# Optimization experiments

Hardware: AMD Instinct MI355X
Metric: run time of the kernel (lower is better)

The kernel has to match this reference:

```python
import jax, jax.numpy as jnp
import numpy as np

B, N, F = 4, 1024, 512        # batch, tokens, features
H, D = 8, 64                  # heads, attention_dim (= value dim here)
E = 16                        # edge feature dim
LN_EPS = 1e-5


def setup_inputs() -> dict:
    key = jax.random.key(0)
    ks = jax.random.split(key, 9)
    receiver_input = jax.random.normal(ks[0], (B, N, F), dtype=jnp.float32)
    edge_features = jax.random.normal(ks[1], (B, N, N, E), dtype=jnp.float32)
    mask = (jax.random.uniform(ks[2], (B, N, N)) > 0.5).astype(jnp.float32)
    s = 1.0 / np.sqrt(F)
    Wq = jax.random.normal(ks[3], (F, H * D), dtype=jnp.float32) * s
    Wk = jax.random.normal(ks[4], (F, H * D), dtype=jnp.float32) * s
    Wv = jax.random.normal(ks[5], (F, H * D), dtype=jnp.float32) * s
    We = jax.random.normal(ks[6], (E, H), dtype=jnp.float32) * (1.0 / np.sqrt(E))
    Wo = jax.random.normal(ks[7], (H * D, H * D), dtype=jnp.float32) * (1.0 / np.sqrt(H * D))
    ln_scale = jnp.ones((F,), dtype=jnp.float32)
    ln_offset = jnp.zeros((F,), dtype=jnp.float32)
    return {
        "receiver_input": receiver_input, "edge_features": edge_features,
        "mask": mask, "ln_scale": ln_scale, "ln_offset": ln_offset,
        "Wq": Wq, "Wk": Wk, "Wv": Wv, "We": We, "Wo": Wo,
    }


def _layer_norm(x, scale, offset):
    mu = jnp.mean(x, axis=-1, keepdims=True)
    var = jnp.var(x, axis=-1, keepdims=True)
    return (x - mu) * jax.lax.rsqrt(var + LN_EPS) * scale + offset


def reference(receiver_input, edge_features, mask, ln_scale, ln_offset, Wq, Wk, Wv, We, Wo):
    r = _layer_norm(receiver_input, ln_scale, ln_offset)   # sender = receiver (self-attn)
    q = (r @ Wq).reshape(B, N, H, D)
    k = (r @ Wk).reshape(B, N, H, D)
    v = (r @ Wv).reshape(B, N, H, D)
    # logits [b, i, j, h]; edge bias added BEFORE softmax (over senders j = axis -2)
    logits = jnp.einsum("bihf,bjhf->bijh", q, k) + edge_features @ We
    w = jax.nn.softmax(logits, axis=-2)
    w = w * mask[..., None]                                 # post-softmax mask multiply
    out = jnp.einsum("bijh,bjhv->bihv", w, v)
    out = out.reshape(B, N, H * D) * (1.0 / jnp.sqrt(jnp.float32(D)))
    out = out @ Wo
    out = out + receiver_input                              # residual (shapes match: F == H*D)
    return out
```

## Files before the change

kernel.cpp:

```cpp
#include <hip/hip_runtime.h>

#define BB 4
#define NN 1024
#define FF 512
#define HH 8
#define DD 64
#define EE 16

typedef unsigned short u16;
typedef _Float16 f16;
typedef __attribute__((ext_vector_type(8))) _Float16 f16x8;
typedef __attribute__((ext_vector_type(4))) _Float16 f16x4;
typedef __attribute__((ext_vector_type(4))) float     f32x4;

#define MFMAH(a,b,c) __builtin_amdgcn_mfma_f32_16x16x32_f16((a),(b),(c),0,0,0)

static __device__ __forceinline__ void gld16(const void* g, void* l){
  __builtin_amdgcn_global_load_lds((const __attribute__((address_space(1))) unsigned int*)g,
                                   (__attribute__((address_space(3))) unsigned int*)l, 16, 0, 0);
}

__global__ __launch_bounds__(256) void k_wsplit(
    const float* __restrict__ Wq, const float* __restrict__ Wk,
    const float* __restrict__ Wv, const float* __restrict__ Wo,
    f16* __restrict__ WT, f16* __restrict__ WoT){
  __shared__ float tile[32][33];
  int bid = blockIdx.x, t = threadIdx.x;
  int isA = bid < 768;
  int tb  = isA ? bid : bid - 768;
  int nct = isA ? 48 : 16;
  int ct = tb % nct, ft = tb / nct;
  int c0 = ct * 32, f0 = ft * 32;
  #pragma unroll
  for (int r4 = 0; r4 < 4; r4++){
    int fl = (t >> 5) * 4 + r4, cl = t & 31;
    int f = f0 + fl, c = c0 + cl;
    float v;
    if (isA){
      const float* W = (c < 512) ? Wq : ((c < 1024) ? Wk : Wv);
      v = W[f * 512 + (c & 511)];
    } else {
      v = Wo[f * 512 + c];
    }
    tile[fl][cl] = v;
  }
  __syncthreads();
  #pragma unroll
  for (int r4 = 0; r4 < 4; r4++){
    int cl = (t >> 5) * 4 + r4, fl = t & 31;
    float v = tile[fl][cl];
    int c = c0 + cl, f = f0 + fl;
    if (isA) WT[c * 512 + f]  = (f16)v;
    else     WoT[c * 512 + f] = (f16)v;
  }
}

__global__ __launch_bounds__(256) void k_ln(
    const float* __restrict__ x, const float* __restrict__ gamma,
    const float* __restrict__ beta, f16* __restrict__ rf){
  int row  = blockIdx.x * 4 + (threadIdx.x >> 6);
  int lane = threadIdx.x & 63;
  const float* px = x + (size_t)row * 512 + lane * 8;
  float4 a = *(const float4*)px;
  float4 b = *(const float4*)(px + 4);
  float v[8] = {a.x,a.y,a.z,a.w,b.x,b.y,b.z,b.w};
  float s = 0.f, q = 0.f;
  #pragma unroll
  for (int j = 0; j < 8; j++){ s += v[j]; q += v[j]*v[j]; }
  #pragma unroll
  for (int m = 1; m < 64; m <<= 1){ s += __shfl_xor(s, m, 64); q += __shfl_xor(q, m, 64); }
  float mean = s * (1.f/512.f);
  float var  = q * (1.f/512.f) - mean * mean;
  float rstd = rsqrtf(var + 1e-5f);
  float4 ga = *(const float4*)(gamma + lane*8);
  float4 gb = *(const float4*)(gamma + lane*8 + 4);
  float4 b0 = *(const float4*)(beta  + lane*8);
  float4 b1 = *(const float4*)(beta  + lane*8 + 4);
  float gs[8] = {ga.x,ga.y,ga.z,ga.w,gb.x,gb.y,gb.z,gb.w};
  float bs[8] = {b0.x,b0.y,b0.z,b0.w,b1.x,b1.y,b1.z,b1.w};
  f16x8 hv;
  #pragma unroll
  for (int j = 0; j < 8; j++){
    float r = (v[j] - mean) * rstd * gs[j] + bs[j];
    hv[j] = (f16)r;
  }
  *(f16x8*)(rf + (size_t)row * 512 + lane * 8) = hv;
}

__global__ __launch_bounds__(256) void k_qkv(
    const f16* __restrict__ rf, const f16* __restrict__ WT,
    f16* __restrict__ qf, f16* __restrict__ kf, f16* __restrict__ vT){
  __shared__ f16 As[128*32], Bs[128*32];
  int bid = blockIdx.x;
  int mt = bid & 31, nt = bid >> 5;
  int m0 = mt << 7,  n0 = nt << 7;
  int t = threadIdx.x, lane = t & 63, w = t >> 6;
  int wm = (w >> 1) << 6, wn = (w & 1) << 6;
  int fr = lane & 15, g = lane >> 4;
  f32x4 acc[4][4];
  #pragma unroll
  for (int i = 0; i < 4; i++)
    #pragma unroll
    for (int j = 0; j < 4; j++) acc[i][j] = (f32x4){0.f,0.f,0.f,0.f};

  for (int k0 = 0; k0 < 512; k0 += 32){
    #pragma unroll
    for (int q = 0; q < 2; q++){
      int c = ((q << 2) + w) * 64 + lane;
      int row = c >> 2, part = c & 3;
      int ldso = ((q << 2) + w) * 512;
      gld16(rf + (size_t)(m0+row)*512 + k0 + part*8, &As[ldso]);
      gld16(WT + (size_t)(n0+row)*512 + k0 + part*8, &Bs[ldso]);
    }
    __syncthreads();
    f16x8 a[4], b[4];
    #pragma unroll
    for (int mi = 0; mi < 4; mi++) a[mi] = *(const f16x8*)&As[(wm + mi*16 + fr)*32 + g*8];
    #pragma unroll
    for (int ni = 0; ni < 4; ni++) b[ni] = *(const f16x8*)&Bs[(wn + ni*16 + fr)*32 + g*8];
    #pragma unroll
    for (int mi = 0; mi < 4; mi++)
      #pragma unroll
      for (int ni = 0; ni < 4; ni++)
        acc[mi][ni] = MFMAH(a[mi], b[ni], acc[mi][ni]);
    __syncthreads();
  }
  #pragma unroll
  for (int mi = 0; mi < 4; mi++)
    #pragma unroll
    for (int ni = 0; ni < 4; ni++)
      #pragma unroll
      for (int r = 0; r < 4; r++){
        int gm = m0 + wm + mi*16 + g*4 + r;
        int gc = n0 + wn + ni*16 + fr;
        float vv = acc[mi][ni][r];
        int b = gm >> 10, i = gm & 1023;
        int mat = gc >> 9, h = (gc >> 6) & 7, d = gc & 63;
        size_t idx = ((size_t)((b << 3) + h) * 1024 + i) * 64 + d;
        if      (mat == 0) qf[idx] = (f16)vv;
        else if (mat == 1) kf[idx] = (f16)vv;
        else vT[((size_t)((b << 3) + h) * 64 + d) * 1024 + i] = (f16)vv;
      }
}

__global__ __launch_bounds__(256) void k_bias(
    const float* __restrict__ edge, const float* __restrict__ We,
    f16* __restrict__ biasP){
  __shared__ char outb[4][1280];
  int t = threadIdx.x, lane = t & 63, w = t >> 6;
  int c = lane & 3, vq = lane >> 2;
  float wr[4][8];
  #pragma unroll
  for (int r = 0; r < 4; r++){
    float4 wa = *(const float4*)(We + (c*4 + r)*8);
    float4 wb = *(const float4*)(We + (c*4 + r)*8 + 4);
    wr[r][0]=wa.x; wr[r][1]=wa.y; wr[r][2]=wa.z; wr[r][3]=wa.w;
    wr[r][4]=wb.x; wr[r][5]=wb.y; wr[r][6]=wb.z; wr[r][7]=wb.w;
  }
  int bid = blockIdx.x;
  int i = bid & 1023, b = bid >> 10;
  const float* erow = edge + (size_t)bid * 16384;
  int h = lane >> 3, vb = lane & 7;
  f16* obase = biasP + (size_t)(b*8 + h) * 1048576 + (size_t)i * 1024;

  auto process = [&](const float4* e, int bt){
    #pragma unroll
    for (int n = 0; n < 4; n++){
      float p[8];
      #pragma unroll
      for (int hh = 0; hh < 8; hh++)
        p[hh] = e[n].x*wr[0][hh] + e[n].y*wr[1][hh] + e[n].z*wr[2][hh] + e[n].w*wr[3][hh];
      #pragma unroll
      for (int hh = 0; hh < 8; hh++){
        p[hh] += __shfl_xor(p[hh], 1, 64);
        p[hh] += __shfl_xor(p[hh], 2, 64);
      }
      unsigned lo = (unsigned)__builtin_bit_cast(u16, (f16)p[2*c]);
      unsigned hi = (unsigned)__builtin_bit_cast(u16, (f16)p[2*c + 1]);
      *(unsigned*)(&outb[w][(n*16 + vq)*20 + c*4]) = lo | (hi << 16);
    }
    asm volatile("s_waitcnt lgkmcnt(0)" ::: "memory");
    __builtin_amdgcn_sched_barrier(0);
    f16x8 ov;
    #pragma unroll
    for (int q = 0; q < 8; q++)
      ov[q] = __builtin_bit_cast(f16, *(const u16*)(&outb[w][(vb*8 + q)*20 + h*2]));
    *(f16x8*)(obase + (w*16 + bt*4)*16 + vb*8) = ov;
    asm volatile("s_waitcnt lgkmcnt(0)" ::: "memory");
    __builtin_amdgcn_sched_barrier(0);
  };

  float4 eA[4], eB[4];
  #pragma unroll
  for (int n = 0; n < 4; n++)
    eA[n] = *(const float4*)(erow + (size_t)(w*16 + n)*256 + lane*4);
  #pragma unroll
  for (int n = 0; n < 4; n++)
    eB[n] = *(const float4*)(erow + (size_t)(w*16 + 4 + n)*256 + lane*4);
  process(eA, 0);
  #pragma unroll
  for (int n = 0; n < 4; n++)
    eA[n] = *(const float4*)(erow + (size_t)(w*16 + 8 + n)*256 + lane*4);
  process(eB, 1);
  #pragma unroll
  for (int n = 0; n < 4; n++)
    eB[n] = *(const float4*)(erow + (size_t)(w*16 + 12 + n)*256 + lane*4);
  process(eA, 2);
  process(eB, 3);
}

__global__ __launch_bounds__(256) void k_attn(
    const f16* __restrict__ biasP, const float* __restrict__ mask,
    const f16* __restrict__ qf, const f16* __restrict__ kf,
    const f16* __restrict__ vT, f16* __restrict__ part_o,
    float2* __restrict__ part_md){
  __shared__ f16 pm_s[4][16*40];
  int t = threadIdx.x, lane = t & 63, w = t >> 6;
  int wid = blockIdx.x * 4 + w;
  int s = wid & 1, it = (wid >> 1) & 63, h = (wid >> 7) & 7, b = wid >> 10;
  int fr = lane & 15, g = lane >> 4;
  int bh = b*8 + h;

  size_t qb = ((size_t)bh * 1024 + it*16 + fr) * 64 + g*8;
  f16x8 qf0 = *(const f16x8*)(qf + qb);
  f16x8 qf1 = *(const f16x8*)(qf + qb + 32);

  const f16*   bbase = biasP + ((size_t)bh * 1024 + it*16) * 1024;
  const float* mbase = mask + (size_t)(b*1024 + it*16) * 1024;
  const f16*   kbase = kf + (size_t)bh * 65536;
  const f16*   vbase = vT + (size_t)bh * 65536;

  f32x4 oacc[4];
  #pragma unroll
  for (int vf = 0; vf < 4; vf++) oacc[vf] = (f32x4){0.f,0.f,0.f,0.f};
  float mrun[4], den[4];
  #pragma unroll
  for (int r = 0; r < 4; r++){ mrun[r] = -3e38f; den[r] = 0.f; }

  #pragma unroll 1
  for (int jt = s*16; jt < s*16 + 16; jt++){
    int j0 = jt << 5;
    const f16* kp = kbase + (size_t)(j0 + fr) * 64 + g*8;
    f16x8 kf00 = *(const f16x8*)(kp);
    f16x8 kf01 = *(const f16x8*)(kp + 32);
    f16x8 kf10 = *(const f16x8*)(kp + 16*64);
    f16x8 kf11 = *(const f16x8*)(kp + 16*64 + 32);
    f16x8 vfr[4];
    #pragma unroll
    for (int vf = 0; vf < 4; vf++)
      vfr[vf] = *(const f16x8*)(vbase + (size_t)(vf*16 + fr) * 1024 + j0 + g*8);
    float bs0[4], bs1[4], ms0[4], ms1[4];
    #pragma unroll
    for (int r = 0; r < 4; r++){
      int row = g*4 + r;
      bs0[r] = (float)bbase[(size_t)row*1024 + j0 + fr];
      bs1[r] = (float)bbase[(size_t)row*1024 + j0 + 16 + fr];
      ms0[r] = mbase[(size_t)row*1024 + j0 + fr];
      ms1[r] = mbase[(size_t)row*1024 + j0 + 16 + fr];
    }

    f32x4 lg0 = (f32x4){0.f,0.f,0.f,0.f};
    f32x4 lg1 = (f32x4){0.f,0.f,0.f,0.f};
    lg0 = MFMAH(qf0, kf00, lg0); lg1 = MFMAH(qf0, kf10, lg1);
    lg0 = MFMAH(qf1, kf01, lg0); lg1 = MFMAH(qf1, kf11, lg1);

    float tm[4];
    #pragma unroll
    for (int r = 0; r < 4; r++){
      lg0[r] += bs0[r];
      lg1[r] += bs1[r];
      tm[r] = fmaxf(lg0[r], lg1[r]);
    }
    #pragma unroll
    for (int mk = 1; mk < 16; mk <<= 1){
      #pragma unroll
      for (int r = 0; r < 4; r++) tm[r] = fmaxf(tm[r], __shfl_xor(tm[r], mk, 16));
    }
    float p0[4], p1[4], scl[4], ps[4];
    #pragma unroll
    for (int r = 0; r < 4; r++){
      float nm = fmaxf(mrun[r], tm[r]);
      scl[r] = exp2f((mrun[r] - nm) * 1.44269504089f);
      mrun[r] = nm;
      p0[r] = exp2f((lg0[r] - nm) * 1.44269504089f);
      p1[r] = exp2f((lg1[r] - nm) * 1.44269504089f);
      ps[r] = p0[r] + p1[r];
    }
    #pragma unroll
    for (int mk = 1; mk < 16; mk <<= 1){
      #pragma unroll
      for (int r = 0; r < 4; r++) ps[r] += __shfl_xor(ps[r], mk, 16);
    }
    #pragma unroll
    for (int r = 0; r < 4; r++) den[r] = den[r] * scl[r] + ps[r];
    #pragma unroll
    for (int vf = 0; vf < 4; vf++)
      #pragma unroll
      for (int r = 0; r < 4; r++) oacc[vf][r] *= scl[r];

    #pragma unroll
    for (int r = 0; r < 4; r++){
      int row = g*4 + r;
      pm_s[w][row*40 + fr]      = (f16)(p0[r] * ms0[r]);
      pm_s[w][row*40 + 16 + fr] = (f16)(p1[r] * ms1[r]);
    }
    asm volatile("s_waitcnt lgkmcnt(0)" ::: "memory");
    f16x8 pa = *(const f16x8*)&pm_s[w][fr*40 + g*8];
    #pragma unroll
    for (int vf = 0; vf < 4; vf++)
      oacc[vf] = MFMAH(pa, vfr[vf], oacc[vf]);
  }

  float id[4];
  #pragma unroll
  for (int r = 0; r < 4; r++) id[r] = 1.0f / den[r];
  #pragma unroll
  for (int vf = 0; vf < 4; vf++)
    #pragma unroll
    for (int r = 0; r < 4; r++){
      int row = g*4 + r;
      part_o[((size_t)((s*32 + bh) * 1024) + it*16 + row) * 64 + vf*16 + fr] =
          (f16)(oacc[vf][r] * id[r]);
    }
  if (fr == 0){
    #pragma unroll
    for (int r = 0; r < 4; r++){
      int row = g*4 + r;
      part_md[(size_t)(s*32 + bh) * 1024 + it*16 + row] = make_float2(mrun[r], den[r]);
    }
  }
}

__global__ __launch_bounds__(256) void k_combine(
    const f16* __restrict__ part_o, const float2* __restrict__ part_md,
    f16* __restrict__ AO){
  int wg   = blockIdx.x * 4 + (threadIdx.x >> 6);
  int lane = threadIdx.x & 63;
  int bh = wg >> 10, i = wg & 1023;
  int b = bh >> 3, h = bh & 7;
  float2 md[2];
  float M = -3e38f;
  #pragma unroll
  for (int s = 0; s < 2; s++){
    md[s] = part_md[(size_t)(s*32 + bh) * 1024 + i];
    M = fmaxf(M, md[s].x);
  }
  float wsum = 0.f, o = 0.f;
  #pragma unroll
  for (int s = 0; s < 2; s++){
    float wq = md[s].y * exp2f((md[s].x - M) * 1.44269504089f);
    wsum += wq;
    o += wq * (float)part_o[((size_t)((s*32 + bh) * 1024) + i) * 64 + lane];
  }
  AO[((size_t)(b*1024 + i)) * 512 + h*64 + lane] = (f16)(o * 0.125f / wsum);
}

__global__ __launch_bounds__(256) void k_out(
    const f16* __restrict__ AO, const f16* __restrict__ WoT,
    const float* __restrict__ x, float* __restrict__ out){
  __shared__ f16 As[64*32], Bs[128*32];
  int bid = blockIdx.x;
  int mt = bid & 63, nt = bid >> 6;
  int m0 = mt << 6, n0 = nt << 7;
  int t = threadIdx.x, lane = t & 63, w = t >> 6;
  int wm = (w >> 1) << 5, wn = (w & 1) << 6;
  int fr = lane & 15, g = lane >> 4;
  f32x4 acc[2][4];
  #pragma unroll
  for (int i = 0; i < 2; i++)
    #pragma unroll
    for (int j = 0; j < 4; j++) acc[i][j] = (f32x4){0.f,0.f,0.f,0.f};

  for (int k0 = 0; k0 < 512; k0 += 32){
    {
      int row = t >> 2, part = t & 3;
      gld16(AO + (size_t)(m0+row)*512 + k0 + part*8, &As[w*512]);
    }
    #pragma unroll
    for (int q = 0; q < 2; q++){
      int c = ((q << 2) + w) * 64 + lane;
      int row = c >> 2, part = c & 3;
      gld16(WoT + (size_t)(n0+row)*512 + k0 + part*8, &Bs[((q<<2)+w)*512]);
    }
    __syncthreads();
    f16x8 af[2], bf_[4];
    #pragma unroll
    for (int mi = 0; mi < 2; mi++) af[mi]  = *(const f16x8*)&As[(wm + mi*16 + fr)*32 + g*8];
    #pragma unroll
    for (int ni = 0; ni < 4; ni++) bf_[ni] = *(const f16x8*)&Bs[(wn + ni*16 + fr)*32 + g*8];
    #pragma unroll
    for (int mi = 0; mi < 2; mi++)
      #pragma unroll
      for (int ni = 0; ni < 4; ni++)
        acc[mi][ni] = MFMAH(af[mi], bf_[ni], acc[mi][ni]);
    __syncthreads();
  }
  #pragma unroll
  for (int mi = 0; mi < 2; mi++)
    #pragma unroll
    for (int ni = 0; ni < 4; ni++)
      #pragma unroll
      for (int r = 0; r < 4; r++){
        size_t gm = m0 + wm + mi*16 + g*4 + r;
        size_t gn = n0 + wn + ni*16 + fr;
        out[gm*512 + gn] = acc[mi][ni][r] + x[gm*512 + gn];
      }
}

extern "C" void kernel_launch(void* const* d_in, const int* in_sizes, int n_in,
                              void* d_out, int out_size, void* d_ws, size_t ws_size,
                              hipStream_t stream){
  const float* xin   = (const float*)d_in[0];
  const float* edge  = (const float*)d_in[1];
  const float* mask  = (const float*)d_in[2];
  const float* gamma = (const float*)d_in[3];
  const float* beta  = (const float*)d_in[4];
  const float* Wq    = (const float*)d_in[5];
  const float* Wk    = (const float*)d_in[6];
  const float* Wv    = (const float*)d_in[7];
  const float* We    = (const float*)d_in[8];
  const float* Wo    = (const float*)d_in[9];
  float* out = (float*)d_out;

  f16* p   = (f16*)d_ws;
  f16* WT      = p;   p += 1536*512;
  f16* WoT     = p;   p += 512*512;
  f16* rf      = p;   p += 4096*512;
  f16* qf      = p;   p += 2097152;
  f16* kf      = p;   p += 2097152;
  f16* vT      = p;   p += 2097152;
  f16* biasP   = p;   p += 33554432;
  f16* part_o  = p;   p += 4194304;
  float2* part_md = (float2*)p;
  f16* AO      = rf;

  k_wsplit <<<1024, 256, 0, stream>>>(Wq, Wk, Wv, Wo, WT, WoT);
  k_ln     <<<1024, 256, 0, stream>>>(xin, gamma, beta, rf);
  k_qkv    <<<384,  256, 0, stream>>>(rf, WT, qf, kf, vT);
  k_bias   <<<4096, 256, 0, stream>>>(edge, We, biasP);
  k_attn   <<<1024, 256, 0, stream>>>(biasP, mask, qf, kf, vT, part_o, part_md);
  k_combine<<<8192, 256, 0, stream>>>(part_o, part_md, AO);
  k_out    <<<256,  256, 0, stream>>>(AO, WoT, xin, out);
}
```

Measured before the change: 190.8 us.

## Merge independent kernels and fold split-K combine into output GEMM

Result: faster. 174.0 us, median of 2 (-8.8%).

```diff
diff --git a/kernel.cpp b/kernel.cpp
--- a/kernel.cpp
+++ b/kernel.cpp
@@ -20,193 +20,193 @@
                                    (__attribute__((address_space(3))) unsigned int*)l, 16, 0, 0);
 }
 
-__global__ __launch_bounds__(256) void k_wsplit(
+__global__ __launch_bounds__(256) void k_prep(
     const float* __restrict__ Wq, const float* __restrict__ Wk,
     const float* __restrict__ Wv, const float* __restrict__ Wo,
-    f16* __restrict__ WT, f16* __restrict__ WoT){
+    const float* __restrict__ x, const float* __restrict__ gamma,
+    const float* __restrict__ beta,
+    f16* __restrict__ WT, f16* __restrict__ WoT, f16* __restrict__ rf){
   __shared__ float tile[32][33];
   int bid = blockIdx.x, t = threadIdx.x;
-  int isA = bid < 768;
-  int tb  = isA ? bid : bid - 768;
-  int nct = isA ? 48 : 16;
-  int ct = tb % nct, ft = tb / nct;
-  int c0 = ct * 32, f0 = ft * 32;
-  #pragma unroll
-  for (int r4 = 0; r4 < 4; r4++){
-    int fl = (t >> 5) * 4 + r4, cl = t & 31;
-    int f = f0 + fl, c = c0 + cl;
-    float v;
-    if (isA){
-      const float* W = (c < 512) ? Wq : ((c < 1024) ? Wk : Wv);
-      v = W[f * 512 + (c & 511)];
-    } else {
-      v = Wo[f * 512 + c];
-    }
-    tile[fl][cl] = v;
+  if (bid < 1024){
+    int isA = bid < 768;
+    int tb  = isA ? bid : bid - 768;
+    int nct = isA ? 48 : 16;
+    int ct = tb % nct, ft = tb / nct;
+    int c0 = ct * 32, f0 = ft * 32;
+    #pragma unroll
+    for (int r4 = 0; r4 < 4; r4++){
+      int fl = (t >> 5) * 4 + r4, cl = t & 31;
+      int f = f0 + fl, c = c0 + cl;
+      float v;
+      if (isA){
+        const float* W = (c < 512) ? Wq : ((c < 1024) ? Wk : Wv);
+        v = W[f * 512 + (c & 511)];
+      } else {
+        v = Wo[f * 512 + c];
+      }
+      tile[fl][cl] = v;
+    }
+    __syncthreads();
+    #pragma unroll
+    for (int r4 = 0; r4 < 4; r4++){
+      int cl = (t >> 5) * 4 + r4, fl = t & 31;
+      float v = tile[fl][cl];
+      int c = c0 + cl, f = f0 + fl;
+      if (isA) WT[c * 512 + f]  = (f16)v;
+      else     WoT[c * 512 + f] = (f16)v;
+    }
+  } else {
+    int row  = (bid - 1024) * 4 + (t >> 6);
+    int lane = t & 63;
+    const float* px = x + (size_t)row * 512 + lane * 8;
+    float4 a = *(const float4*)px;
+    float4 b = *(const float4*)(px + 4);
+    float v[8] = {a.x,a.y,a.z,a.w,b.x,b.y,b.z,b.w};
+    float s = 0.f, q = 0.f;
+    #pragma unroll
+    for (int j = 0; j < 8; j++){ s += v[j]; q += v[j]*v[j]; }
+    #pragma unroll
+    for (int m = 1; m < 64; m <<= 1){ s += __shfl_xor(s, m, 64); q += __shfl_xor(q, m, 64); }
+    float mean = s * (1.f/512.f);
+    float var  = q * (1.f/512.f) - mean * mean;
+    float rstd = rsqrtf(var + 1e-5f);
+    float4 ga = *(const float4*)(gamma + lane*8);
+    float4 gb = *(const float4*)(gamma + lane*8 + 4);
+    float4 b0 = *(const float4*)(beta  + lane*8);
+    float4 b1 = *(const float4*)(beta  + lane*8 + 4);
+    float gs[8] = {ga.x,ga.y,ga.z,ga.w,gb.x,gb.y,gb.z,gb.w};
+    float bs[8] = {b0.x,b0.y,b0.z,b0.w,b1.x,b1.y,b1.z,b1.w};
+    f16x8 hv;
+    #pragma unroll
+    for (int j = 0; j < 8; j++){
+      float r = (v[j] - mean) * rstd * gs[j] + bs[j];
+      hv[j] = (f16)r;
+    }
+    *(f16x8*)(rf + (size_t)row * 512 + lane * 8) = hv;
   }
-  __syncthreads();
-  #pragma unroll
-  for (int r4 = 0; r4 < 4; r4++){
-    int cl = (t >> 5) * 4 + r4, fl = t & 31;
-    float v = tile[fl][cl];
-    int c = c0 + cl, f = f0 + fl;
-    if (isA) WT[c * 512 + f]  = (f16)v;
-    else     WoT[c * 512 + f] = (f16)v;
-  }
-}
-
-__global__ __launch_bounds__(256) void k_ln(
-    const float* __restrict__ x, const float* __restrict__ gamma,
-    const float* __restrict__ beta, f16* __restrict__ rf){
-  int row  = blockIdx.x * 4 + (threadIdx.x >> 6);
-  int lane = threadIdx.x & 63;
-  const float* px = x + (size_t)row * 512 + lane * 8;
-  float4 a = *(const float4*)px;
-  float4 b = *(const float4*)(px + 4);
-  float v[8] = {a.x,a.y,a.z,a.w,b.x,b.y,b.z,b.w};
-  float s = 0.f, q = 0.f;
-  #pragma unroll
-  for (int j = 0; j < 8; j++){ s += v[j]; q += v[j]*v[j]; }
-  #pragma unroll
-  for (int m = 1; m < 64; m <<= 1){ s += __shfl_xor(s, m, 64); q += __shfl_xor(q, m, 64); }
-  float mean = s * (1.f/512.f);
-  float var  = q * (1.f/512.f) - mean * mean;
-  float rstd = rsqrtf(var + 1e-5f);
-  float4 ga = *(const float4*)(gamma + lane*8);
-  float4 gb = *(const float4*)(gamma + lane*8 + 4);
-  float4 b0 = *(const float4*)(beta  + lane*8);
-  float4 b1 = *(const float4*)(beta  + lane*8 + 4);
-  float gs[8] = {ga.x,ga.y,ga.z,ga.w,gb.x,gb.y,gb.z,gb.w};
-  float bs[8] = {b0.x,b0.y,b0.z,b0.w,b1.x,b1.y,b1.z,b1.w};
-  f16x8 hv;
-  #pragma unroll
-  for (int j = 0; j < 8; j++){
-    float r = (v[j] - mean) * rstd * gs[j] + bs[j];
-    hv[j] = (f16)r;
-  }
-  *(f16x8*)(rf + (size_t)row * 512 + lane * 8) = hv;
-}
-
-__global__ __launch_bounds__(256) void k_qkv(
+}
+
+__global__ __launch_bounds__(256) void k_bq(
     const f16* __restrict__ rf, const f16* __restrict__ WT,
-    f16* __restrict__ qf, f16* __restrict__ kf, f16* __restrict__ vT){
-  __shared__ f16 As[128*32], Bs[128*32];
-  int bid = blockIdx.x;
-  int mt = bid & 31, nt = bid >> 5;
-  int m0 = mt << 7,  n0 = nt << 7;
-  int t = threadIdx.x, lane = t & 63, w = t >> 6;
-  int wm = (w >> 1) << 6, wn = (w & 1) << 6;
-  int fr = lane & 15, g = lane >> 4;
-  f32x4 acc[4][4];
-  #pragma unroll
-  for (int i = 0; i < 4; i++)
-    #pragma unroll
-    for (int j = 0; j < 4; j++) acc[i][j] = (f32x4){0.f,0.f,0.f,0.f};
-
-  for (int k0 = 0; k0 < 512; k0 += 32){
-    #pragma unroll
-    for (int q = 0; q < 2; q++){
-      int c = ((q << 2) + w) * 64 + lane;
-      int row = c >> 2, part = c & 3;
-      int ldso = ((q << 2) + w) * 512;
-      gld16(rf + (size_t)(m0+row)*512 + k0 + part*8, &As[ldso]);
-      gld16(WT + (size_t)(n0+row)*512 + k0 + part*8, &Bs[ldso]);
-    }
-    __syncthreads();
-    f16x8 a[4], b[4];
-    #pragma unroll
-    for (int mi = 0; mi < 4; mi++) a[mi] = *(const f16x8*)&As[(wm + mi*16 + fr)*32 + g*8];
-    #pragma unroll
-    for (int ni = 0; ni < 4; ni++) b[ni] = *(const f16x8*)&Bs[(wn + ni*16 + fr)*32 + g*8];
-    #pragma unroll
-    for (int mi = 0; mi < 4; mi++)
-      #pragma unroll
-      for (int ni = 0; ni < 4; ni++)
-        acc[mi][ni] = MFMAH(a[mi], b[ni], acc[mi][ni]);
-    __syncthreads();
-  }
-  #pragma unroll
-  for (int mi = 0; mi < 4; mi++)
-    #pragma unroll
-    for (int ni = 0; ni < 4; ni++)
-      #pragma unroll
-      for (int r = 0; r < 4; r++){
-        int gm = m0 + wm + mi*16 + g*4 + r;
-        int gc = n0 + wn + ni*16 + fr;
-        float vv = acc[mi][ni][r];
-        int b = gm >> 10, i = gm & 1023;
-        int mat = gc >> 9, h = (gc >> 6) & 7, d = gc & 63;
-        size_t idx = ((size_t)((b << 3) + h) * 1024 + i) * 64 + d;
-        if      (mat == 0) qf[idx] = (f16)vv;
-        else if (mat == 1) kf[idx] = (f16)vv;
-        else vT[((size_t)((b << 3) + h) * 64 + d) * 1024 + i] = (f16)vv;
-      }
-}
-
-__global__ __launch_bounds__(256) void k_bias(
+    f16* __restrict__ qf, f16* __restrict__ kf, f16* __restrict__ vT,
     const float* __restrict__ edge, const float* __restrict__ We,
     f16* __restrict__ biasP){
+  __shared__ f16 As[128*32], Bs[128*32];
   __shared__ char outb[4][1280];
   int t = threadIdx.x, lane = t & 63, w = t >> 6;
-  int c = lane & 3, vq = lane >> 2;
-  float wr[4][8];
-  #pragma unroll
-  for (int r = 0; r < 4; r++){
-    float4 wa = *(const float4*)(We + (c*4 + r)*8);
-    float4 wb = *(const float4*)(We + (c*4 + r)*8 + 4);
-    wr[r][0]=wa.x; wr[r][1]=wa.y; wr[r][2]=wa.z; wr[r][3]=wa.w;
-    wr[r][4]=wb.x; wr[r][5]=wb.y; wr[r][6]=wb.z; wr[r][7]=wb.w;
+
+  if (blockIdx.x < 384){
+    int bid = blockIdx.x;
+    int mt = bid & 31, nt = bid >> 5;
+    int m0 = mt << 7,  n0 = nt << 7;
+    int wm = (w >> 1) << 6, wn = (w & 1) << 6;
+    int fr = lane & 15, g = lane >> 4;
+    f32x4 acc[4][4];
+    #pragma unroll
+    for (int i = 0; i < 4; i++)
+      #pragma unroll
+      for (int j = 0; j < 4; j++) acc[i][j] = (f32x4){0.f,0.f,0.f,0.f};
+
+    for (int k0 = 0; k0 < 512; k0 += 32){
+      #pragma unroll
+      for (int q = 0; q < 2; q++){
+        int c = ((q << 2) + w) * 64 + lane;
+        int row = c >> 2, part = c & 3;
+        int ldso = ((q << 2) + w) * 512;
+        gld16(rf + (size_t)(m0+row)*512 + k0 + part*8, &As[ldso]);
+        gld16(WT + (size_t)(n0+row)*512 + k0 + part*8, &Bs[ldso]);
+      }
+      __syncthreads();
+      f16x8 a[4], b[4];
+      #pragma unroll
+      for (int mi = 0; mi < 4; mi++) a[mi] = *(const f16x8*)&As[(wm + mi*16 + fr)*32 + g*8];
+      #pragma unroll
+      for (int ni = 0; ni < 4; ni++) b[ni] = *(const f16x8*)&Bs[(wn + ni*16 + fr)*32 + g*8];
+      #pragma unroll
+      for (int mi = 0; mi < 4; mi++)
+        #pragma unroll
+        for (int ni = 0; ni < 4; ni++)
+          acc[mi][ni] = MFMAH(a[mi], b[ni], acc[mi][ni]);
+      __syncthreads();
+    }
+    #pragma unroll
+    for (int mi = 0; mi < 4; mi++)
+      #pragma unroll
+      for (int ni = 0; ni < 4; ni++)
+        #pragma unroll
+        for (int r = 0; r < 4; r++){
+          int gm = m0 + wm + mi*16 + g*4 + r;
+          int gc = n0 + wn + ni*16 + fr;
+          float vv = acc[mi][ni][r];
+          int b = gm >> 10, i = gm & 1023;
+          int mat = gc >> 9, h = (gc >> 6) & 7, d = gc & 63;
+          size_t idx = ((size_t)((b << 3) + h) * 1024 + i) * 64 + d;
+          if      (mat == 0) qf[idx] = (f16)vv;
+          else if (mat == 1) kf[idx] = (f16)vv;
+          else vT[((size_t)((b << 3) + h) * 64 + d) * 1024 + i] = (f16)vv;
+        }
+  } else {
+    int bid = blockIdx.x - 384;
+    int c = lane & 3, vq = lane >> 2;
+    float wr[4][8];
+    #pragma unroll
+    for (int r = 0; r < 4; r++){
+      float4 wa = *(const float4*)(We + (c*4 + r)*8);
+      float4 wb = *(const float4*)(We + (c*4 + r)*8 + 4);
+      wr[r][0]=wa.x; wr[r][1]=wa.y; wr[r][2]=wa.z; wr[r][3]=wa.w;
+      wr[r][4]=wb.x; wr[r][5]=wb.y; wr[r][6]=wb.z; wr[r][7]=wb.w;
+    }
+    int i = bid & 1023, b = bid >> 10;
+    const float* erow = edge + (size_t)bid * 16384;
+    int h = lane >> 3, vb = lane & 7;
+    f16* obase = biasP + (size_t)(b*8 + h) * 1048576 + (size_t)i * 1024;
+
+    auto process = [&](const float4* e, int bt){
+      #pragma unroll
+      for (int n = 0; n < 4; n++){
+        float p[8];
+        #pragma unroll
+        for (int hh = 0; hh < 8; hh++)
+          p[hh] = e[n].x*wr[0][hh] + e[n].y*wr[1][hh] + e[n].z*wr[2][hh] + e[n].w*wr[3][hh];
+        #pragma unroll
+        for (int hh = 0; hh < 8; hh++){
+          p[hh] += __shfl_xor(p[hh], 1, 64);
+          p[hh] += __shfl_xor(p[hh], 2, 64);
+        }
+        unsigned lo = (unsigned)__builtin_bit_cast(u16, (f16)p[2*c]);
+        unsigned hi = (unsigned)__builtin_bit_cast(u16, (f16)p[2*c + 1]);
+        *(unsigned*)(&outb[w][(n*16 + vq)*20 + c*4]) = lo | (hi << 16);
+      }
+      asm volatile("s_waitcnt lgkmcnt(0)" ::: "memory");
+      __builtin_amdgcn_sched_barrier(0);
+      f16x8 ov;
+      #pragma unroll
+      for (int q = 0; q < 8; q++)
+        ov[q] = __builtin_bit_cast(f16, *(const u16*)(&outb[w][(vb*8 + q)*20 + h*2]));
+      *(f16x8*)(obase + (w*16 + bt*4)*16 + vb*8) = ov;
+      asm volatile("s_waitcnt lgkmcnt(0)" ::: "memory");
+      __builtin_amdgcn_sched_barrier(0);
+    };
+
+    float4 eA[4], eB[4];
+    #pragma unroll
+    for (int n = 0; n < 4; n++)
+      eA[n] = *(const float4*)(erow + (size_t)(w*16 + n)*256 + lane*4);
+    #pragma unroll
+    for (int n = 0; n < 4; n++)
+      eB[n] = *(const float4*)(erow + (size_t)(w*16 + 4 + n)*256 + lane*4);
+    process(eA, 0);
+    #pragma unroll
+    for (int n = 0; n < 4; n++)
+      eA[n] = *(const float4*)(erow + (size_t)(w*16 + 8 + n)*256 + lane*4);
+    process(eB, 1);
+    #pragma unroll
+    for (int n = 0; n < 4; n++)
+      eB[n] = *(const float4*)(erow + (size_t)(w*16 + 12 + n)*256 + lane*4);
+    process(eA, 2);
+    process(eB, 3);
   }
-  int bid = blockIdx.x;
-  int i = bid & 1023, b = bid >> 10;
-  const float* erow = edge + (size_t)bid * 16384;
-  int h = lane >> 3, vb = lane & 7;
-  f16* obase = biasP + (size_t)(b*8 + h) * 1048576 + (size_t)i * 1024;
-
-  auto process = [&](const float4* e, int bt){
-    #pragma unroll
-    for (int n = 0; n < 4; n++){
-      float p[8];
-      #pragma unroll
-      for (int hh = 0; hh < 8; hh++)
-        p[hh] = e[n].x*wr[0][hh] + e[n].y*wr[1][hh] + e[n].z*wr[2][hh] + e[n].w*wr[3][hh];
-      #pragma unroll
-      for (int hh = 0; hh < 8; hh++){
-        p[hh] += __shfl_xor(p[hh], 1, 64);
-        p[hh] += __shfl_xor(p[hh], 2, 64);
-      }
-      unsigned lo = (unsigned)__builtin_bit_cast(u16, (f16)p[2*c]);
-      unsigned hi = (unsigned)__builtin_bit_cast(u16, (f16)p[2*c + 1]);
-      *(unsigned*)(&outb[w][(n*16 + vq)*20 + c*4]) = lo | (hi << 16);
-    }
-    asm volatile("s_waitcnt lgkmcnt(0)" ::: "memory");
-    __builtin_amdgcn_sched_barrier(0);
-    f16x8 ov;
-    #pragma unroll
-    for (int q = 0; q < 8; q++)
-      ov[q] = __builtin_bit_cast(f16, *(const u16*)(&outb[w][(vb*8 + q)*20 + h*2]));
-    *(f16x8*)(obase + (w*16 + bt*4)*16 + vb*8) = ov;
-    asm volatile("s_waitcnt lgkmcnt(0)" ::: "memory");
-    __builtin_amdgcn_sched_barrier(0);
-  };
-
-  float4 eA[4], eB[4];
-  #pragma unroll
-  for (int n = 0; n < 4; n++)
-    eA[n] = *(const float4*)(erow + (size_t)(w*16 + n)*256 + lane*4);
-  #pragma unroll
-  for (int n = 0; n < 4; n++)
-    eB[n] = *(const float4*)(erow + (size_t)(w*16 + 4 + n)*256 + lane*4);
-  process(eA, 0);
-  #pragma unroll
-  for (int n = 0; n < 4; n++)
-    eA[n] = *(const float4*)(erow + (size_t)(w*16 + 8 + n)*256 + lane*4);
-  process(eB, 1);
-  #pragma unroll
-  for (int n = 0; n < 4; n++)
-    eB[n] = *(const float4*)(erow + (size_t)(w*16 + 12 + n)*256 + lane*4);
-  process(eA, 2);
-  process(eB, 3);
 }
 
 __global__ __launch_bounds__(256) void k_attn(
@@ -331,32 +331,9 @@
   }
 }
 
-__global__ __launch_bounds__(256) void k_combine(
+__global__ __launch_bounds__(256) void k_out(
     const f16* __restrict__ part_o, const float2* __restrict__ part_md,
-    f16* __restrict__ AO){
-  int wg   = blockIdx.x * 4 + (threadIdx.x >> 6);
-  int lane = threadIdx.x & 63;
-  int bh = wg >> 10, i = wg & 1023;
-  int b = bh >> 3, h = bh & 7;
-  float2 md[2];
-  float M = -3e38f;
-  #pragma unroll
-  for (int s = 0; s < 2; s++){
-    md[s] = part_md[(size_t)(s*32 + bh) * 1024 + i];
-    M = fmaxf(M, md[s].x);
-  }
-  float wsum = 0.f, o = 0.f;
-  #pragma unroll
-  for (int s = 0; s < 2; s++){
-    float wq = md[s].y * exp2f((md[s].x - M) * 1.44269504089f);
-    wsum += wq;
-    o += wq * (float)part_o[((size_t)((s*32 + bh) * 1024) + i) * 64 + lane];
-  }
-  AO[((size_t)(b*1024 + i)) * 512 + h*64 + lane] = (f16)(o * 0.125f / wsum);
-}
-
-__global__ __launch_bounds__(256) void k_out(
-    const f16* __restrict__ AO, const f16* __restrict__ WoT,
+    const f16* __restrict__ WoT,
     const float* __restrict__ x, float* __restrict__ out){
   __shared__ f16 As[64*32], Bs[128*32];
   int bid = blockIdx.x;
@@ -371,16 +348,34 @@
     #pragma unroll
     for (int j = 0; j < 4; j++) acc[i][j] = (f32x4){0.f,0.f,0.f,0.f};
 
+  int row_l = t >> 2, part = t & 3;
+  int grow = m0 + row_l;
+  int b = grow >> 10, i = grow & 1023;
+
   for (int k0 = 0; k0 < 512; k0 += 32){
     {
-      int row = t >> 2, part = t & 3;
-      gld16(AO + (size_t)(m0+row)*512 + k0 + part*8, &As[w*512]);
+      int col0 = k0 + part*8;
+      int h = col0 >> 6, d0 = col0 & 63;
+      int bh = b*8 + h;
+      float2 md0 = part_md[(size_t)bh * 1024 + i];
+      float2 md1 = part_md[(size_t)(32 + bh) * 1024 + i];
+      float M = fmaxf(md0.x, md1.x);
+      float w0 = md0.y * exp2f((md0.x - M) * 1.44269504089f);
+      float w1 = md1.y * exp2f((md1.x - M) * 1.44269504089f);
+      float scl = 0.125f / (w0 + w1);
+      f16x8 a0 = *(const f16x8*)(part_o + ((size_t)bh * 1024 + i) * 64 + d0);
+      f16x8 a1 = *(const f16x8*)(part_o + ((size_t)(32 + bh) * 1024 + i) * 64 + d0);
+      f16x8 av;
+      #pragma unroll
+      for (int dd = 0; dd < 8; dd++)
+        av[dd] = (f16)(((float)a0[dd] * w0 + (float)a1[dd] * w1) * scl);
+      *(f16x8*)&As[row_l*32 + part*8] = av;
     }
     #pragma unroll
     for (int q = 0; q < 2; q++){
       int c = ((q << 2) + w) * 64 + lane;
-      int row = c >> 2, part = c & 3;
-      gld16(WoT + (size_t)(n0+row)*512 + k0 + part*8, &Bs[((q<<2)+w)*512]);
+      int row = c >> 2, prt = c & 3;
+      gld16(WoT + (size_t)(n0+row)*512 + k0 + prt*8, &Bs[((q<<2)+w)*512]);
     }
     __syncthreads();
     f16x8 af[2], bf_[4];
@@ -432,13 +427,9 @@
   f16* biasP   = p;   p += 33554432;
   f16* part_o  = p;   p += 4194304;
   float2* part_md = (float2*)p;
-  f16* AO      = rf;
-
-  k_wsplit <<<1024, 256, 0, stream>>>(Wq, Wk, Wv, Wo, WT, WoT);
-  k_ln     <<<1024, 256, 0, stream>>>(xin, gamma, beta, rf);
-  k_qkv    <<<384,  256, 0, stream>>>(rf, WT, qf, kf, vT);
-  k_bias   <<<4096, 256, 0, stream>>>(edge, We, biasP);
-  k_attn   <<<1024, 256, 0, stream>>>(biasP, mask, qf, kf, vT, part_o, part_md);
-  k_combine<<<8192, 256, 0, stream>>>(part_o, part_md, AO);
-  k_out    <<<256,  256, 0, stream>>>(AO, WoT, xin, out);
-}
+
+  k_prep <<<2048, 256, 0, stream>>>(Wq, Wk, Wv, Wo, xin, gamma, beta, WT, WoT, rf);
+  k_bq   <<<4480, 256, 0, stream>>>(rf, WT, qf, kf, vT, edge, We, biasP);
+  k_attn <<<1024, 256, 0, stream>>>(biasP, mask, qf, kf, vT, part_o, part_md);
+  k_out  <<<256,  256, 0, stream>>>(part_o, part_md, WoT, xin, out);
+}
```
